# Optimization experiments

Hardware: AMD Instinct MI355X
Metric: run time of the kernel (lower is better)

## Reference

```python
import jax, jax.numpy as jnp
import numpy as np

N_NODES = 50000
N_EDGES = 1600000
IN_DIM, HIDDEN, OUT_DIM = 128, 128, 64


def setup_inputs() -> dict:
    key = jax.random.key(0)
    ks = jax.random.split(key, 8)
    x = jax.random.normal(ks[0], (N_NODES, IN_DIM), dtype=jnp.float32)
    edge_index = jax.random.randint(ks[1], (2, N_EDGES), 0, N_NODES, dtype=jnp.int64)
    # SAGEConv params: lin_l applied to aggregated neighbors (with bias),
    # lin_r applied to root/self features (no bias) -- PyG defaults.
    def lin_init(k, fan_in, fan_out):
        bound = 1.0 / np.sqrt(fan_in)
        return jax.random.uniform(k, (fan_in, fan_out), jnp.float32, -bound, bound)
    W1_l = lin_init(ks[2], IN_DIM, HIDDEN)
    W1_r = lin_init(ks[3], IN_DIM, HIDDEN)
    b1 = jnp.zeros((HIDDEN,), jnp.float32)
    W2_l = lin_init(ks[4], HIDDEN, OUT_DIM)
    W2_r = lin_init(ks[5], HIDDEN, OUT_DIM)
    b2 = jnp.zeros((OUT_DIM,), jnp.float32)
    return {"x": x, "edge_index": edge_index, "W1_l": W1_l, "W1_r": W1_r,
            "b1": b1, "W2_l": W2_l, "W2_r": W2_r, "b2": b2}


def _sage_conv(h, src, dst, n_nodes, W_l, W_r, b):
    # gather messages from source nodes, mean-aggregate at destinations
    msg = h[src]                                              # [E, D]
    agg_sum = jax.ops.segment_sum(msg, dst, num_segments=n_nodes)
    deg = jax.ops.segment_sum(jnp.ones((src.shape[0],), h.dtype), dst,
                              num_segments=n_nodes)
    agg_mean = agg_sum / jnp.maximum(deg, 1.0)[:, None]       # [N, D]
    return agg_mean @ W_l + h @ W_r + b


def reference(x, edge_index, W1_l, W1_r, b1, W2_l, W2_r, b2):
    n = x.shape[0]
    src, dst = edge_index[0], edge_index[1]
    h = jax.nn.relu(_sage_conv(x, src, dst, n, W1_l, W1_r, b1))
    return _sage_conv(h, src, dst, n, W2_l, W2_r, b2)
```

## Files before the change

kernel.cpp:

```cpp
#include <hip/hip_runtime.h>

#define NN 50000
#define NE 1600000
#define BSTRIDE 96
#define BNODES 50
#define C_BKT 1000
#define P1_BLKS 128
#define P1_CHUNK 12500
#define XCVT_BLKS 1563
#define WCVT_BLKS 48
#define PP_PREP (XCVT_BLKS + WCVT_BLKS)
#define RGRP 3128

typedef __bf16 bf16x8 __attribute__((ext_vector_type(8)));
typedef float  f32x4  __attribute__((ext_vector_type(4)));
typedef float  f32x2  __attribute__((ext_vector_type(2)));

__device__ __forceinline__ float bfLo(uint u) { union { uint i; float f; } v; v.i = u << 16; return v.f; }
__device__ __forceinline__ float bfHi(uint u) { union { uint i; float f; } v; v.i = u & 0xffff0000u; return v.f; }
__device__ __forceinline__ ushort f2bf(float f) {
    union { float f; uint i; } v; v.f = f;
    uint r = v.i + 0x7fffu + ((v.i >> 16) & 1u);
    return (ushort)(r >> 16);
}
__device__ __forceinline__ uint pack2(float a, float b) {
    return (uint)f2bf(a) | ((uint)f2bf(b) << 16);
}
__device__ __forceinline__ bf16x8 load8(const ushort* p) {
    union { uint4 u; bf16x8 b; } v; v.u = *(const uint4*)p; return v.b;
}

#define ACC8(u) { a0 += bfLo(u.x); a1 += bfHi(u.x); a2 += bfLo(u.y); a3 += bfHi(u.y); \
                  a4 += bfLo(u.z); a5 += bfHi(u.z); a6 += bfLo(u.w); a7 += bfHi(u.w); }

#define CVA(u, o) { f32x2 p0 = __builtin_amdgcn_cvt_pk_f32_fp8((int)(u), 0); \
                    f32x2 p1 = __builtin_amdgcn_cvt_pk_f32_fp8((int)(u), 1); \
                    a[(o)+0] += p0.x; a[(o)+1] += p0.y; a[(o)+2] += p1.x; a[(o)+3] += p1.y; }
#define ACCF8(v) { CVA((v).x, 0); CVA((v).y, 4); CVA((v).z, 8); CVA((v).w, 12); }

__device__ __forceinline__ int pkOff(int n, int k) {
    return (((n >> 4) * 4 + (k >> 5)) * 512) + (((k >> 3) & 3) * 128) + ((n & 15) * 8) + (k & 7);
}

__global__ __launch_bounds__(1024) void k_pp(
    const float4* __restrict__ x, ushort* __restrict__ xbp, uint* __restrict__ xf8,
    const float* __restrict__ W1l, const float* __restrict__ W1r,
    const float* __restrict__ W2l, const float* __restrict__ W2r,
    ushort* __restrict__ T1l, ushort* __restrict__ T1r,
    ushort* __restrict__ T2l, ushort* __restrict__ T2r,
    const int* __restrict__ src, const int* __restrict__ dst,
    uint* __restrict__ cells, uint* __restrict__ offc) {
    __shared__ uint hist[C_BKT + 1];
    __shared__ uint part[128];
    const int b = blockIdx.x;
    const int tid = threadIdx.x;
    if (b < XCVT_BLKS) {
        int i = b * 1024 + tid;
        if (i < NN * 128 / 4) {
            float4 v = x[i];
            int r = i >> 5, k0 = (i & 31) * 4;
            ushort4 o; o.x = f2bf(v.x); o.y = f2bf(v.y); o.z = f2bf(v.z); o.w = f2bf(v.w);
            *(ushort4*)(xbp + pkOff(r, k0)) = o;
            uint rr = (uint)__builtin_amdgcn_cvt_pk_fp8_f32(v.x, v.y, 0, 0);
            rr = (uint)__builtin_amdgcn_cvt_pk_fp8_f32(v.z, v.w, (int)rr, 1);
            xf8[i] = rr;
        }
    } else if (b < PP_PREP) {
        int i = (b - XCVT_BLKS) * 1024 + tid;
        if (i < 16384) {
            int k = i >> 7, n = i & 127; T1l[pkOff(n, k)] = f2bf(W1l[i]);
        } else if (i < 32768) {
            int j = i - 16384; int k = j >> 7, n = j & 127; T1r[pkOff(n, k)] = f2bf(W1r[j]);
        } else if (i < 40960) {
            int j = i - 32768; int k = j >> 6, n = j & 63;  T2l[pkOff(n, k)] = f2bf(W2l[j]);
        } else {
            int j = i - 40960; int k = j >> 6, n = j & 63;  T2r[pkOff(n, k)] = f2bf(W2r[j]);
        }
    } else {
        const int b2 = b - PP_PREP;
        for (int i = tid; i < C_BKT; i += 1024) hist[i] = 0;
        __syncthreads();
        const int beg = b2 * P1_CHUNK;
        for (int i = beg + tid; i < beg + P1_CHUNK; i += 1024) {
            int c = dst[i] / BNODES;
            atomicAdd(&hist[c], 1);
        }
        __syncthreads();
        if (tid < 125) {
            uint s = 0;
            #pragma unroll
            for (int k = 0; k < 8; k++) {
                uint t = hist[tid * 8 + k];
                hist[tid * 8 + k] = s;
                s += t;
            }
            part[tid] = s;
        }
        __syncthreads();
        if (tid == 0) {
            uint run = 0;
            for (int t = 0; t < 125; t++) { uint tmp = part[t]; part[t] = run; run += tmp; }
        }
        __syncthreads();
        if (tid < 125) {
            uint bs = part[tid];
            if (bs) {
                #pragma unroll
                for (int k = 0; k < 8; k++) hist[tid * 8 + k] += bs;
            }
        }
        __syncthreads();
        for (int c = tid; c < C_BKT; c += 1024) {
            uint st = hist[c];
            uint en = (c == C_BKT - 1) ? (uint)P1_CHUNK : hist[c + 1];
            offc[(size_t)b2 * C_BKT + c] = st | ((en - st) << 16);
        }
        __syncthreads();
        uint* myCells = cells + (size_t)b2 * P1_CHUNK;
        for (int i = beg + tid; i < beg + P1_CHUNK; i += 1024) {
            int d = dst[i];
            int s = src[i];
            int c = d / BNODES;
            uint p = atomicAdd(&hist[c], 1);
            myCells[p] = ((uint)(d - c * BNODES) << 16) | (uint)s;
        }
    }
}

__global__ __launch_bounds__(512) void k_pagg(
    const uint* __restrict__ cells, const uint* __restrict__ offc,
    const uchar* __restrict__ xf8, ushort* __restrict__ col,
    int* __restrict__ deg, ushort* __restrict__ aggp) {
    __shared__ uint hist[BNODES];
    __shared__ __align__(16) ushort colS[BNODES * BSTRIDE];
    const int bid = blockIdx.x;
    const int c = (bid & 7) * 125 + (bid >> 3);
    const int tid = threadIdx.x;
    if (tid < BNODES) hist[tid] = 0;
    __syncthreads();
    {
        const int b = tid >> 2, sub = tid & 3;
        uint v = offc[(size_t)b * C_BKT + c];
        int st = (int)(v & 0xFFFF), n = (int)(v >> 16);
        const uint* cell = cells + (size_t)b * P1_CHUNK + st;
        for (int j = sub; j < n; j += 4) {
            uint e = cell[j];
            int dl = e >> 16;
            uint p = atomicAdd(&hist[dl], 1);
            if (p < BSTRIDE) colS[dl * BSTRIDE + p] = (ushort)(e & 0xFFFF);
        }
    }
    __syncthreads();
    const int nodeBase = c * BNODES;
    if (tid < BNODES) deg[nodeBase + tid] = (int)hist[tid];
    {
        uint4* cg = (uint4*)(col + (size_t)nodeBase * BSTRIDE);
        const uint4* cs = (const uint4*)colS;
        for (int i = tid; i < BNODES * BSTRIDE / 8; i += 512) cg[i] = cs[i];
    }
    const int wave = tid >> 6, lane = tid & 63;
    const int q = lane >> 3;
    const int cc = lane & 7;
    for (int ln = wave; ln < BNODES; ln += 8) {
        int d = (int)hist[ln];
        int dd = min(d, BSTRIDE);
        const ushort* cb = &colS[ln * BSTRIDE];
        float a[16];
        #pragma unroll
        for (int i = 0; i < 16; i++) a[i] = 0.f;
        for (int j0 = 0; j0 < dd; j0 += 64) {
            int idx = (j0 + lane < dd) ? (int)cb[j0 + lane] : 0;
            int cnt2 = min(64, dd - j0);
            int t = 0;
            for (; t + 32 <= cnt2; t += 32) {
                int s0 = __shfl(idx, t + q);
                int s1 = __shfl(idx, t + 8 + q);
                int s2 = __shfl(idx, t + 16 + q);
                int s3 = __shfl(idx, t + 24 + q);
                uint4 u0 = *(const uint4*)(xf8 + (size_t)s0 * 128 + cc * 16);
                uint4 u1 = *(const uint4*)(xf8 + (size_t)s1 * 128 + cc * 16);
                uint4 u2 = *(const uint4*)(xf8 + (size_t)s2 * 128 + cc * 16);
                uint4 u3 = *(const uint4*)(xf8 + (size_t)s3 * 128 + cc * 16);
                ACCF8(u0); ACCF8(u1); ACCF8(u2); ACCF8(u3);
            }
            for (; t + 16 <= cnt2; t += 16) {
                int s0 = __shfl(idx, t + q);
                int s1 = __shfl(idx, t + 8 + q);
                uint4 u0 = *(const uint4*)(xf8 + (size_t)s0 * 128 + cc * 16);
                uint4 u1 = *(const uint4*)(xf8 + (size_t)s1 * 128 + cc * 16);
                ACCF8(u0); ACCF8(u1);
            }
            for (; t < cnt2; t += 8) {
                int s = __shfl(idx, t + q);
                if (t + q < cnt2) {
                    uint4 u = *(const uint4*)(xf8 + (size_t)s * 128 + cc * 16);
                    ACCF8(u);
                }
            }
        }
        #pragma unroll
        for (int m = 8; m < 64; m <<= 1) {
            #pragma unroll
            for (int i = 0; i < 16; i++) a[i] += __shfl_xor(a[i], m);
        }
        if (q == 0) {
            int node = nodeBase + ln;
            float inv = 1.f / fmaxf((float)d, 1.f);
            int base = ((node >> 4) * 4 + (cc >> 1)) * 512 + ((cc & 1) * 2) * 128 + (node & 15) * 8;
            uint4 o;
            o.x = pack2(a[0] * inv, a[1] * inv);
            o.y = pack2(a[2] * inv, a[3] * inv);
            o.z = pack2(a[4] * inv, a[5] * inv);
            o.w = pack2(a[6] * inv, a[7] * inv);
            *(uint4*)(aggp + base) = o;
            o.x = pack2(a[8] * inv, a[9] * inv);
            o.y = pack2(a[10] * inv, a[11] * inv);
            o.z = pack2(a[12] * inv, a[13] * inv);
            o.w = pack2(a[14] * inv, a[15] * inv);
            *(uint4*)(aggp + base + 128) = o;
        }
    }
}

#define PAD1 136
__global__ __launch_bounds__(256) void k_gemm12(
    const ushort* __restrict__ aggp, const ushort* __restrict__ xbp,
    const ushort* __restrict__ T1l, const ushort* __restrict__ T1r,
    const ushort* __restrict__ T2l, const ushort* __restrict__ T2r,
    const float* __restrict__ b1, const float* __restrict__ b2,
    ushort* __restrict__ hW, float* __restrict__ outp) {
    __shared__ ushort hS[2][16 * PAD1];
    const int lane = threadIdx.x & 63;
    const int wave = threadIdx.x >> 6;
    const int s = wave >> 1;
    const int ch = wave & 1;
    const int quad = lane >> 4, r16 = lane & 15;
    const int row0 = blockIdx.x * 32 + s * 16;
    const int g = blockIdx.x * 2 + s;
    ushort* myS = &hS[s][0];

    f32x4 acc[4];
    #pragma unroll
    for (int nt = 0; nt < 4; nt++) acc[nt] = (f32x4){0.f, 0.f, 0.f, 0.f};
    #pragma unroll
    for (int kt = 0; kt < 4; kt++) {
        bf16x8 aAgg = load8(aggp + (size_t)(g * 4 + kt) * 512 + lane * 8);
        bf16x8 aXb  = load8(xbp  + (size_t)(g * 4 + kt) * 512 + lane * 8);
        #pragma unroll
        for (int nt = 0; nt < 4; nt++) {
            const int tile = ((ch * 4 + nt) * 4 + kt) * 512 + lane * 8;
            acc[nt] = __builtin_amdgcn_mfma_f32_16x16x32_bf16(aAgg, load8(T1l + tile), acc[nt], 0, 0, 0);
            acc[nt] = __builtin_amdgcn_mfma_f32_16x16x32_bf16(aXb,  load8(T1r + tile), acc[nt], 0, 0, 0);
        }
    }
    #pragma unroll
    for (int nt = 0; nt < 4; nt++) {
        int cc = ch * 64 + nt * 16 + r16;
        float bv = b1[cc];
        #pragma unroll
        for (int i = 0; i < 4; i++)
            myS[(quad * 4 + i) * PAD1 + cc] = f2bf(fmaxf(acc[nt][i] + bv, 0.f));
    }
    __syncthreads();

    f32x4 acc2[2], acc3[2];
    #pragma unroll
    for (int nt = 0; nt < 2; nt++) {
        acc2[nt] = (f32x4){0.f, 0.f, 0.f, 0.f};
        acc3[nt] = (f32x4){0.f, 0.f, 0.f, 0.f};
    }
    #pragma unroll
    for (int kt = 0; kt < 4; kt++) {
        bf16x8 ah = load8(&myS[r16 * PAD1 + kt * 32 + quad * 8]);
        #pragma unroll
        for (int nt = 0; nt < 2; nt++) {
            const int tile = ((ch * 2 + nt) * 4 + kt) * 512 + lane * 8;
            acc2[nt] = __builtin_amdgcn_mfma_f32_16x16x32_bf16(ah, load8(T2l + tile), acc2[nt], 0, 0, 0);
            acc3[nt] = __builtin_amdgcn_mfma_f32_16x16x32_bf16(ah, load8(T2r + tile), acc3[nt], 0, 0, 0);
        }
    }
    #pragma unroll
    for (int nt = 0; nt < 2; nt++) {
        int cc = ch * 32 + nt * 16 + r16;
        float bv = b2[cc];
        #pragma unroll
        for (int i = 0; i < 4; i++) {
            int rr = row0 + quad * 4 + i;
            if (rr < NN) {
                hW[(size_t)rr * 64 + cc] = f2bf(acc2[nt][i]);
                outp[(size_t)rr * 64 + cc] = acc3[nt][i] + bv;
            }
        }
    }
}

__global__ void k_agg64f(const ushort* __restrict__ hW, const ushort* __restrict__ col,
                         const int* __restrict__ deg, const float* __restrict__ outp,
                         float* __restrict__ out) {
    int node = (blockIdx.x * blockDim.x + threadIdx.x) >> 6;
    int lane = threadIdx.x & 63;
    int q = lane >> 3;
    int c = lane & 7;
    int d = deg[node];
    int dd = min(d, BSTRIDE);
    const ushort* cb = col + (size_t)node * BSTRIDE;
    float a0=0.f,a1=0.f,a2=0.f,a3=0.f,a4=0.f,a5=0.f,a6=0.f,a7=0.f;
    for (int j0 = 0; j0 < dd; j0 += 64) {
        int idx = (j0 + lane < dd) ? (int)cb[j0 + lane] : 0;
        int cnt = min(64, dd - j0);
        int t = 0;
        for (; t + 16 <= cnt; t += 16) {
            int s0 = __shfl(idx, t + q);
            int s1 = __shfl(idx, t + 8 + q);
            uint4 u0 = *(const uint4*)(hW + (size_t)s0 * 64 + c * 8);
            uint4 u1 = *(const uint4*)(hW + (size_t)s1 * 64 + c * 8);
            ACC8(u0); ACC8(u1);
        }
        for (; t < cnt; t += 8) {
            int s = __shfl(idx, t + q);
            if (t + q < cnt) {
                uint4 u = *(const uint4*)(hW + (size_t)s * 64 + c * 8);
                ACC8(u);
            }
        }
    }
    #pragma unroll
    for (int m = 8; m < 64; m <<= 1) {
        a0 += __shfl_xor(a0, m); a1 += __shfl_xor(a1, m);
        a2 += __shfl_xor(a2, m); a3 += __shfl_xor(a3, m);
        a4 += __shfl_xor(a4, m); a5 += __shfl_xor(a5, m);
        a6 += __shfl_xor(a6, m); a7 += __shfl_xor(a7, m);
    }
    if (q == 0) {
        float inv = 1.f / fmaxf((float)d, 1.f);
        float4 p0 = *(const float4*)(outp + (size_t)node * 64 + c * 8);
        float4 p1 = *(const float4*)(outp + (size_t)node * 64 + c * 8 + 4);
        float4 o;
        o.x = a0 * inv + p0.x; o.y = a1 * inv + p0.y;
        o.z = a2 * inv + p0.z; o.w = a3 * inv + p0.w;
        *(float4*)(out + (size_t)node * 64 + c * 8) = o;
        o.x = a4 * inv + p1.x; o.y = a5 * inv + p1.y;
        o.z = a6 * inv + p1.z; o.w = a7 * inv + p1.w;
        *(float4*)(out + (size_t)node * 64 + c * 8 + 4) = o;
    }
}

extern "C" void kernel_launch(void* const* d_in, const int* in_sizes, int n_in,
                              void* d_out, int out_size, void* d_ws, size_t ws_size,
                              hipStream_t stream) {
    const float* x   = (const float*)d_in[0];
    const int*   ei  = (const int*)d_in[1];
    const float* W1l = (const float*)d_in[2];
    const float* W1r = (const float*)d_in[3];
    const float* b1  = (const float*)d_in[4];
    const float* W2l = (const float*)d_in[5];
    const float* W2r = (const float*)d_in[6];
    const float* b2  = (const float*)d_in[7];
    float* out = (float*)d_out;

    const int* src = ei;
    const int* dst = ei + NE;

    char* w = (char*)d_ws;
    ushort* col   = (ushort*)w;                  w += (size_t)NN * BSTRIDE * 2;
    int* deg      = (int*)w;                     w += (size_t)50048 * 4;
    uint* offc    = (uint*)w;                    w += (size_t)P1_BLKS * C_BKT * 4;
    ushort* xbp   = (ushort*)w;                  w += (size_t)RGRP * 2048 * 2;
    ushort* T1l   = (ushort*)w;                  w += 128 * 128 * 2;
    ushort* T1r   = (ushort*)w;                  w += 128 * 128 * 2;
    ushort* T2l   = (ushort*)w;                  w += 64 * 128 * 2;
    ushort* T2r   = (ushort*)w;                  w += 64 * 128 * 2;
    ushort* aggp  = (ushort*)w;                  w += (size_t)RGRP * 2048 * 2;
    ushort* hW    = (ushort*)w;                  w += (size_t)NN * 64 * 2;
    float* outp   = (float*)w;                   w += (size_t)NN * 64 * 4;
    uchar* xf8    = (uchar*)w;                   w += (size_t)NN * 128;
    uint* cells   = (uint*)w;                    w += (size_t)NE * 4;

    k_pp<<<PP_PREP + P1_BLKS, 1024, 0, stream>>>(
        (const float4*)x, xbp, (uint*)xf8, W1l, W1r, W2l, W2r,
        T1l, T1r, T2l, T2r, src, dst, cells, offc);

    k_pagg<<<C_BKT, 512, 0, stream>>>(cells, offc, xf8, col, deg, aggp);

    k_gemm12<<<(NN + 31) / 32, 256, 0, stream>>>(aggp, xbp, T1l, T1r, T2l, T2r, b1, b2, hW, outp);

    k_agg64f<<<NN / 4, 256, 0, stream>>>(hW, col, deg, outp, out);
}
```

Baseline: 213.0 us.

## Pad neighbor lists with zero-row sentinel and double the edge-bucketing blocks

Neighbor lists are padded to a multiple of 8 with a sentinel index that points to a zeroed row appended to the fp8 and bf16 feature tables. This lets both gather loops read indices straight from shared memory with no shuffles and no per-lane bounds checks. The edge-bucketing phase now uses twice as many blocks with half-sized chunks, and the offset table is transposed so the aggregation kernel reads it contiguously. The layer-2 aggregation now stages its column lists in shared memory per block. The cost is wasted gathers of the zero row for padding slots, plus an extra barrier and slightly larger buffers.

New measurement: 196.0 us. 1.09x faster.

```diff
diff --git a/kernel.cpp b/kernel.cpp
--- a/kernel.cpp
+++ b/kernel.cpp
@@ -5,8 +5,9 @@
 #define BSTRIDE 96
 #define BNODES 50
 #define C_BKT 1000
-#define P1_BLKS 128
-#define P1_CHUNK 12500
+#define P1_BLKS 256
+#define P1_CHUNK 6250
+#define ZID 50000
 #define XCVT_BLKS 1563
 #define WCVT_BLKS 48
 #define PP_PREP (XCVT_BLKS + WCVT_BLKS)
@@ -49,7 +50,7 @@
     ushort* __restrict__ T1l, ushort* __restrict__ T1r,
     ushort* __restrict__ T2l, ushort* __restrict__ T2r,
     const int* __restrict__ src, const int* __restrict__ dst,
-    uint* __restrict__ cells, uint* __restrict__ offc) {
+    uint* __restrict__ cells, uint* __restrict__ offc, ushort* __restrict__ hW) {
     __shared__ uint hist[C_BKT + 1];
     __shared__ uint part[128];
     const int b = blockIdx.x;
@@ -64,6 +65,9 @@
             uint rr = (uint)__builtin_amdgcn_cvt_pk_fp8_f32(v.x, v.y, 0, 0);
             rr = (uint)__builtin_amdgcn_cvt_pk_fp8_f32(v.z, v.w, (int)rr, 1);
             xf8[i] = rr;
+        } else if (b == XCVT_BLKS - 1) {
+            if (tid >= 512 && tid < 544) xf8[(size_t)ZID * 32 + (tid - 512)] = 0;
+            else if (tid >= 544 && tid < 576) ((uint*)hW)[(size_t)ZID * 32 + (tid - 544)] = 0;
         }
     } else if (b < PP_PREP) {
         int i = (b - XCVT_BLKS) * 1024 + tid;
@@ -81,10 +85,8 @@
         for (int i = tid; i < C_BKT; i += 1024) hist[i] = 0;
         __syncthreads();
         const int beg = b2 * P1_CHUNK;
-        for (int i = beg + tid; i < beg + P1_CHUNK; i += 1024) {
-            int c = dst[i] / BNODES;
-            atomicAdd(&hist[c], 1);
-        }
+        for (int i = beg + tid; i < beg + P1_CHUNK; i += 1024)
+            atomicAdd(&hist[dst[i] / BNODES], 1);
         __syncthreads();
         if (tid < 125) {
             uint s = 0;
@@ -113,7 +115,7 @@
         for (int c = tid; c < C_BKT; c += 1024) {
             uint st = hist[c];
             uint en = (c == C_BKT - 1) ? (uint)P1_CHUNK : hist[c + 1];
-            offc[(size_t)b2 * C_BKT + c] = st | ((en - st) << 16);
+            offc[(size_t)c * P1_BLKS + b2] = st | ((en - st) << 16);
         }
         __syncthreads();
         uint* myCells = cells + (size_t)b2 * P1_CHUNK;
@@ -139,11 +141,11 @@
     if (tid < BNODES) hist[tid] = 0;
     __syncthreads();
     {
-        const int b = tid >> 2, sub = tid & 3;
-        uint v = offc[(size_t)b * C_BKT + c];
+        const int b = tid >> 1, sub = tid & 1;
+        uint v = offc[(size_t)c * P1_BLKS + b];
         int st = (int)(v & 0xFFFF), n = (int)(v >> 16);
         const uint* cell = cells + (size_t)b * P1_CHUNK + st;
-        for (int j = sub; j < n; j += 4) {
+        for (int j = sub; j < n; j += 2) {
             uint e = cell[j];
             int dl = e >> 16;
             uint p = atomicAdd(&hist[dl], 1);
@@ -152,7 +154,13 @@
     }
     __syncthreads();
     const int nodeBase = c * BNODES;
-    if (tid < BNODES) deg[nodeBase + tid] = (int)hist[tid];
+    if (tid < BNODES) {
+        deg[nodeBase + tid] = (int)hist[tid];
+        int dd = min((int)hist[tid], BSTRIDE);
+        int dr = (dd + 7) & ~7;
+        for (int j = dd; j < dr; j++) colS[tid * BSTRIDE + j] = (ushort)ZID;
+    }
+    __syncthreads();
     {
         uint4* cg = (uint4*)(col + (size_t)nodeBase * BSTRIDE);
         const uint4* cs = (const uint4*)colS;
@@ -164,39 +172,27 @@
     for (int ln = wave; ln < BNODES; ln += 8) {
         int d = (int)hist[ln];
         int dd = min(d, BSTRIDE);
-        const ushort* cb = &colS[ln * BSTRIDE];
+        int nb = ((dd + 7) & ~7) >> 3;
+        const int base = ln * BSTRIDE;
         float a[16];
         #pragma unroll
         for (int i = 0; i < 16; i++) a[i] = 0.f;
-        for (int j0 = 0; j0 < dd; j0 += 64) {
-            int idx = (j0 + lane < dd) ? (int)cb[j0 + lane] : 0;
-            int cnt2 = min(64, dd - j0);
-            int t = 0;
-            for (; t + 32 <= cnt2; t += 32) {
-                int s0 = __shfl(idx, t + q);
-                int s1 = __shfl(idx, t + 8 + q);
-                int s2 = __shfl(idx, t + 16 + q);
-                int s3 = __shfl(idx, t + 24 + q);
-                uint4 u0 = *(const uint4*)(xf8 + (size_t)s0 * 128 + cc * 16);
-                uint4 u1 = *(const uint4*)(xf8 + (size_t)s1 * 128 + cc * 16);
-                uint4 u2 = *(const uint4*)(xf8 + (size_t)s2 * 128 + cc * 16);
-                uint4 u3 = *(const uint4*)(xf8 + (size_t)s3 * 128 + cc * 16);
-                ACCF8(u0); ACCF8(u1); ACCF8(u2); ACCF8(u3);
-            }
-            for (; t + 16 <= cnt2; t += 16) {
-                int s0 = __shfl(idx, t + q);
-                int s1 = __shfl(idx, t + 8 + q);
-                uint4 u0 = *(const uint4*)(xf8 + (size_t)s0 * 128 + cc * 16);
-                uint4 u1 = *(const uint4*)(xf8 + (size_t)s1 * 128 + cc * 16);
-                ACCF8(u0); ACCF8(u1);
-            }
-            for (; t < cnt2; t += 8) {
-                int s = __shfl(idx, t + q);
-                if (t + q < cnt2) {
-                    uint4 u = *(const uint4*)(xf8 + (size_t)s * 128 + cc * 16);
-                    ACCF8(u);
-                }
-            }
+        int t = 0;
+        for (; t + 4 <= nb; t += 4) {
+            int s0 = (int)colS[base + t * 8 + q];
+            int s1 = (int)colS[base + t * 8 + 8 + q];
+            int s2 = (int)colS[base + t * 8 + 16 + q];
+            int s3 = (int)colS[base + t * 8 + 24 + q];
+            uint4 u0 = *(const uint4*)(xf8 + (size_t)s0 * 128 + cc * 16);
+            uint4 u1 = *(const uint4*)(xf8 + (size_t)s1 * 128 + cc * 16);
+            uint4 u2 = *(const uint4*)(xf8 + (size_t)s2 * 128 + cc * 16);
+            uint4 u3 = *(const uint4*)(xf8 + (size_t)s3 * 128 + cc * 16);
+            ACCF8(u0); ACCF8(u1); ACCF8(u2); ACCF8(u3);
+        }
+        for (; t < nb; t++) {
+            int s = (int)colS[base + t * 8 + q];
+            uint4 u = *(const uint4*)(xf8 + (size_t)s * 128 + cc * 16);
+            ACCF8(u);
         }
         #pragma unroll
         for (int m = 8; m < 64; m <<= 1) {
@@ -206,18 +202,18 @@
         if (q == 0) {
             int node = nodeBase + ln;
             float inv = 1.f / fmaxf((float)d, 1.f);
-            int base = ((node >> 4) * 4 + (cc >> 1)) * 512 + ((cc & 1) * 2) * 128 + (node & 15) * 8;
+            int basep = ((node >> 4) * 4 + (cc >> 1)) * 512 + ((cc & 1) * 2) * 128 + (node & 15) * 8;
             uint4 o;
             o.x = pack2(a[0] * inv, a[1] * inv);
             o.y = pack2(a[2] * inv, a[3] * inv);
             o.z = pack2(a[4] * inv, a[5] * inv);
             o.w = pack2(a[6] * inv, a[7] * inv);
-            *(uint4*)(aggp + base) = o;
+            *(uint4*)(aggp + basep) = o;
             o.x = pack2(a[8] * inv, a[9] * inv);
             o.y = pack2(a[10] * inv, a[11] * inv);
             o.z = pack2(a[12] * inv, a[13] * inv);
             o.w = pack2(a[14] * inv, a[15] * inv);
-            *(uint4*)(aggp + base + 128) = o;
+            *(uint4*)(aggp + basep + 128) = o;
         }
     }
 }
@@ -294,35 +290,43 @@
     }
 }
 
-__global__ void k_agg64f(const ushort* __restrict__ hW, const ushort* __restrict__ col,
-                         const int* __restrict__ deg, const float* __restrict__ outp,
-                         float* __restrict__ out) {
-    int node = (blockIdx.x * blockDim.x + threadIdx.x) >> 6;
-    int lane = threadIdx.x & 63;
-    int q = lane >> 3;
-    int c = lane & 7;
+__global__ __launch_bounds__(256) void k_agg64f(
+    const ushort* __restrict__ hW, const ushort* __restrict__ col,
+    const int* __restrict__ deg, const float* __restrict__ outp,
+    float* __restrict__ out) {
+    __shared__ __align__(16) ushort colB[4 * BSTRIDE];
+    const int tid = threadIdx.x;
+    const int node0 = blockIdx.x * 4;
+    if (tid < 48) {
+        const uint4* cg = (const uint4*)(col + (size_t)node0 * BSTRIDE);
+        *(uint4*)&colB[tid * 8] = cg[tid];
+    }
+    __syncthreads();
+    const int wave = tid >> 6, lane = tid & 63;
+    const int node = node0 + wave;
+    const int q = lane >> 3;
+    const int c = lane & 7;
+    const int base = wave * BSTRIDE;
     int d = deg[node];
     int dd = min(d, BSTRIDE);
-    const ushort* cb = col + (size_t)node * BSTRIDE;
+    int nb = ((dd + 7) & ~7) >> 3;
     float a0=0.f,a1=0.f,a2=0.f,a3=0.f,a4=0.f,a5=0.f,a6=0.f,a7=0.f;
-    for (int j0 = 0; j0 < dd; j0 += 64) {
-        int idx = (j0 + lane < dd) ? (int)cb[j0 + lane] : 0;
-        int cnt = min(64, dd - j0);
-        int t = 0;
-        for (; t + 16 <= cnt; t += 16) {
-            int s0 = __shfl(idx, t + q);
-            int s1 = __shfl(idx, t + 8 + q);
-            uint4 u0 = *(const uint4*)(hW + (size_t)s0 * 64 + c * 8);
-            uint4 u1 = *(const uint4*)(hW + (size_t)s1 * 64 + c * 8);
-            ACC8(u0); ACC8(u1);
-        }
-        for (; t < cnt; t += 8) {
-            int s = __shfl(idx, t + q);
-            if (t + q < cnt) {
-                uint4 u = *(const uint4*)(hW + (size_t)s * 64 + c * 8);
-                ACC8(u);
-            }
-        }
+    int t = 0;
+    for (; t + 4 <= nb; t += 4) {
+        int s0 = (int)colB[base + t * 8 + q];
+        int s1 = (int)colB[base + t * 8 + 8 + q];
+        int s2 = (int)colB[base + t * 8 + 16 + q];
+        int s3 = (int)colB[base + t * 8 + 24 + q];
+        uint4 u0 = *(const uint4*)(hW + (size_t)s0 * 64 + c * 8);
+        uint4 u1 = *(const uint4*)(hW + (size_t)s1 * 64 + c * 8);
+        uint4 u2 = *(const uint4*)(hW + (size_t)s2 * 64 + c * 8);
+        uint4 u3 = *(const uint4*)(hW + (size_t)s3 * 64 + c * 8);
+        ACC8(u0); ACC8(u1); ACC8(u2); ACC8(u3);
+    }
+    for (; t < nb; t++) {
+        int s = (int)colB[base + t * 8 + q];
+        uint4 u = *(const uint4*)(hW + (size_t)s * 64 + c * 8);
+        ACC8(u);
     }
     #pragma unroll
     for (int m = 8; m < 64; m <<= 1) {
@@ -364,21 +368,21 @@
     char* w = (char*)d_ws;
     ushort* col   = (ushort*)w;                  w += (size_t)NN * BSTRIDE * 2;
     int* deg      = (int*)w;                     w += (size_t)50048 * 4;
-    uint* offc    = (uint*)w;                    w += (size_t)P1_BLKS * C_BKT * 4;
+    uint* offc    = (uint*)w;                    w += (size_t)C_BKT * P1_BLKS * 4;
     ushort* xbp   = (ushort*)w;                  w += (size_t)RGRP * 2048 * 2;
     ushort* T1l   = (ushort*)w;                  w += 128 * 128 * 2;
     ushort* T1r   = (ushort*)w;                  w += 128 * 128 * 2;
     ushort* T2l   = (ushort*)w;                  w += 64 * 128 * 2;
     ushort* T2r   = (ushort*)w;                  w += 64 * 128 * 2;
     ushort* aggp  = (ushort*)w;                  w += (size_t)RGRP * 2048 * 2;
-    ushort* hW    = (ushort*)w;                  w += (size_t)NN * 64 * 2;
+    ushort* hW    = (ushort*)w;                  w += (size_t)(NN + 16) * 64 * 2;
     float* outp   = (float*)w;                   w += (size_t)NN * 64 * 4;
-    uchar* xf8    = (uchar*)w;                   w += (size_t)NN * 128;
+    uchar* xf8    = (uchar*)w;                   w += (size_t)(NN + 16) * 128;
     uint* cells   = (uint*)w;                    w += (size_t)NE * 4;
 
     k_pp<<<PP_PREP + P1_BLKS, 1024, 0, stream>>>(
         (const float4*)x, xbp, (uint*)xf8, W1l, W1r, W2l, W2r,
-        T1l, T1r, T2l, T2r, src, dst, cells, offc);
+        T1l, T1r, T2l, T2r, src, dst, cells, offc, hW);
 
     k_pagg<<<C_BKT, 512, 0, stream>>>(cells, offc, xf8, col, deg, aggp);
 
```
